# Optimization experiments

Hardware: AMD Instinct MI355X
Metric: run time of the kernel (lower is better)

Reference implementation:

```python
import jax, jax.numpy as jnp
import numpy as np

EMBED_DIM = 200
INPUT_DIM = 512


def setup_inputs() -> dict:
    key = jax.random.key(0)
    k1, k2, k3, k4 = jax.random.split(key, 4)
    B, L, T = 64, 256, 64
    x = jax.random.normal(k1, (B, L, INPUT_DIM), dtype=jnp.float32)
    y = jax.random.normal(k2, (B, T, INPUT_DIM), dtype=jnp.float32)
    # fc = nn.Linear(input_dim, embedding_dim)
    W = jax.random.normal(k3, (EMBED_DIM, INPUT_DIM), dtype=jnp.float32) * (1.0 / np.sqrt(INPUT_DIM))
    b = jax.random.normal(k4, (EMBED_DIM,), dtype=jnp.float32) * 0.01
    return {"x": x, "y": y, "W": W, "b": b}


def reference(x, y, W, b):
    # Project both modalities (last dim != embedding_dim in original triggers fc)
    xp = jnp.einsum('bld,ed->ble', x, W) + b   # B x L x E
    yp = jnp.einsum('btd,ed->bte', y, W) + b   # B x T x E
    # Pairwise matchmap: for pair (i, j), matchmap = xp[i] @ yp[j].T -> L x T
    mm = jnp.einsum('ile,jte->ijlt', xp, yp)   # B x B x L x T
    # MISA: max over L (rows of matchmap, dim 0), then mean over T
    S = jnp.max(mm, axis=2).mean(axis=2)       # B x B
    return S
```

## Files before the change

### kernel.cpp

```cpp
#include <hip/hip_runtime.h>
#include <hip/hip_bf16.h>
#include <stdint.h>

#define BB 64
#define LL 256
#define TT 64
#define DD 512
#define EE 200
#define EP 208
#define NKK 13
#define NROWS_X 16384
#define BSTRIDE 264
#define PBM 80

typedef __attribute__((ext_vector_type(8))) short short8;
typedef __attribute__((ext_vector_type(4))) float floatx4;
typedef __attribute__((ext_vector_type(16))) float floatx16;

__device__ __forceinline__ short f2bf(float f) {
  uint32_t u = __builtin_bit_cast(uint32_t, f);
  u = (u + 0x7fffu + ((u >> 16) & 1u)) >> 16;
  return (short)u;
}

__device__ __forceinline__ uint32_t pack2(float lo, float hi) {
  return __builtin_amdgcn_perm(__builtin_bit_cast(uint32_t, hi),
                               __builtin_bit_cast(uint32_t, lo), 0x07060302u);
}

typedef const __attribute__((address_space(1))) uint32_t gu32_t;
typedef __attribute__((address_space(3))) uint32_t lu32_t;
__device__ __forceinline__ void glds16(const void* g, void* l) {
  __builtin_amdgcn_global_load_lds((gu32_t*)g, (lu32_t*)l, 16, 0, 0);
}

#define VMCNT_BARRIER(N) asm volatile("s_waitcnt vmcnt(" #N ") lgkmcnt(0)\n\ts_barrier" ::: "memory")

__global__ void wcvt_kernel(const float* __restrict__ W, short* __restrict__ Wb) {
  const int t = blockIdx.x * 256 + threadIdx.x;
  const int base = t * 8;
  const int e = base >> 9;
  short8 o;
  if (e < EE) {
    const floatx4 f0 = *(const floatx4*)(W + base);
    const floatx4 f1 = *(const floatx4*)(W + base + 4);
    o[0] = f2bf(f0.x); o[1] = f2bf(f0.y); o[2] = f2bf(f0.z); o[3] = f2bf(f0.w);
    o[4] = f2bf(f1.x); o[5] = f2bf(f1.y); o[6] = f2bf(f1.z); o[7] = f2bf(f1.w);
  } else {
    o = (short8)0;
  }
  *(short8*)(Wb + base) = o;
}

__global__ __launch_bounds__(960, 1) void proj_kernel(const float* __restrict__ x,
                                                      const float* __restrict__ y,
                                                      const short* __restrict__ Wb,
                                                      const float* __restrict__ bias,
                                                      short* __restrict__ pT) {
  __shared__ __align__(16) char smem[70656];
  float* ldsA = (float*)smem;
  short* ldsB = (short*)(smem + 30720);
  short* bounce = (short*)smem;

  const int tid  = threadIdx.x;
  const int lane = tid & 63;
  const int wid  = tid >> 6;
  const int r16   = lane & 15;
  const int khalf = lane >> 4;
  const int mw = wid % 5;
  const int eh = wid / 5;
  const int nbase = (eh == 0) ? 0 : (eh == 1) ? 5 : 9;
  const int ncnt  = (eh == 0) ? 5 : 4;

  const int row0 = blockIdx.x * PBM;

  floatx4 acc[5];
#pragma unroll
  for (int n = 0; n < 5; n++) acc[n] = (floatx4){0.f, 0.f, 0.f, 0.f};

  auto stage = [&](int buf, int ks) {
    {
      if (tid < 640) {
        const int a = tid;
        const int r = a >> 3, c = a & 7;
        const int gr = row0 + r;
        const float* src = (gr < NROWS_X) ? (x + (size_t)gr * DD)
                                          : (y + (size_t)(gr - NROWS_X) * DD);
        glds16(src + ks * 32 + ((c ^ (r & 7)) << 2),
               &ldsA[buf * 2560 + a * 4]);
      } else {
        const int q = tid - 640;
        const int r = q >> 2, c = q & 3;
        glds16(Wb + (size_t)r * DD + ks * 32 + ((c ^ ((r >> 1) & 3)) << 3),
               &ldsB[buf * 6656 + q * 8]);
      }
    }
    {
      const int q = (tid < 512) ? (tid + 320) : (tid - 512);
      const int r = q >> 2, c = q & 3;
      glds16(Wb + (size_t)r * DD + ks * 32 + ((c ^ ((r >> 1) & 3)) << 3),
             &ldsB[buf * 6656 + q * 8]);
    }
  };

  auto compute = [&](int s) {
    const int buf = s % 3;
    const int r = mw * 16 + r16;
    const int c0 = (2 * khalf) ^ (r & 7);
    const int c1 = (2 * khalf + 1) ^ (r & 7);
    const floatx4 f0 = *(const floatx4*)&ldsA[buf * 2560 + r * 32 + c0 * 4];
    const floatx4 f1 = *(const floatx4*)&ldsA[buf * 2560 + r * 32 + c1 * 4];
    union { short8 s8; uint32_t u[4]; } af;
    af.u[0] = pack2(f0.x, f0.y);
    af.u[1] = pack2(f0.z, f0.w);
    af.u[2] = pack2(f1.x, f1.y);
    af.u[3] = pack2(f1.z, f1.w);
    const int bcol = (khalf ^ ((r16 >> 1) & 3)) << 3;
#pragma unroll
    for (int n = 0; n < 5; n++) {
      if (n < ncnt) {
        const int erow = (nbase + n) * 16 + r16;
        const short8 bfrag = *(const short8*)&ldsB[buf * 6656 + erow * 32 + bcol];
        acc[n] = __builtin_amdgcn_mfma_f32_16x16x32_bf16(af.s8, bfrag, acc[n], 0, 0, 0);
      }
    }
  };

  stage(0, 0);
  stage(1, 1);

  for (int s = 0; s < 15; s++) {
    VMCNT_BARRIER(2);
    if (s + 2 < 16) stage((s + 2) % 3, s + 2);
    compute(s);
  }
  VMCNT_BARRIER(0);
  compute(15);

  __syncthreads();

  for (int n = 0; n < ncnt; n++) {
    const int e = (nbase + n) * 16 + r16;
    const float bv = (e < EE) ? bias[e] : 0.0f;
#pragma unroll
    for (int rr = 0; rr < 4; rr++) {
      const int lr = mw * 16 + khalf * 4 + rr;
      bounce[lr * BSTRIDE + e] = f2bf(acc[n][rr] + bv);
    }
  }
  __syncthreads();

  for (int c = tid; c < 2080; c += 960) {
    const int n    = c / 160;
    const int rem  = c - n * 160;
    const int lrow = rem >> 1;
    const int ehh  = rem & 1;
    const int gr   = row0 + lrow;
    const short8 piece = *(const short8*)&bounce[lrow * BSTRIDE + n * 16 + ehh * 8];
    *(short8*)&pT[((size_t)((gr >> 5) * 13 + n)) * 512 + (size_t)(((ehh << 5) | (gr & 31)) * 8)] = piece;
  }
}

__global__ __launch_bounds__(512, 2) void pair_kernel(const short* __restrict__ xpT,
                                                      const short* __restrict__ ypT,
                                                      float* __restrict__ S) {
  __shared__ __align__(16) char lds[2 * 53248 + 16384];
  float* red = (float*)(lds + 2 * 53248);

  const int tid  = threadIdx.x;
  const int lane = tid & 63;
  const int wid  = tid >> 6;
  const int jj2  = wid >> 2;
  const int wj   = wid & 3;
  const int bid  = blockIdx.x;
  const int i    = bid & 63;
  const int jq   = bid >> 6;
  const int jbase = jq * 16;

  short8 a0[NKK], a1[NKK];
  {
    const short* ab0 = xpT + ((size_t)((i * 8 + wj * 2 + 0) * NKK)) * 512 + lane * 8;
    const short* ab1 = xpT + ((size_t)((i * 8 + wj * 2 + 1) * NKK)) * 512 + lane * 8;
#pragma unroll
    for (int kk = 0; kk < NKK; kk++) {
      a0[kk] = *(const short8*)(ab0 + kk * 512);
      a1[kk] = *(const short8*)(ab1 + kk * 512);
    }
  }

  auto stageB = [&](int g) {
    const short* src = ypT + (size_t)(jbase + g * 2) * 26 * 512;
    char* dst = lds + (g & 1) * 53248;
    for (int c = tid; c < 3328; c += 512)
      glds16(src + (size_t)c * 8, dst + c * 16);
  };

  stageB(0);
  __syncthreads();

  for (int g = 0; g < 8; g++) {
    if (g + 1 < 8) stageB(g + 1);

    const int j = g * 2 + jj2;
    const short* bbase = (const short*)(lds + (g & 1) * 53248) +
                         (size_t)(jj2 * 26 * 512) + lane * 8;

    floatx16 accA0n0, accA0n1, accA1n0, accA1n1;
#pragma unroll
    for (int r = 0; r < 16; r++) {
      accA0n0[r] = 0.f; accA0n1[r] = 0.f; accA1n0[r] = 0.f; accA1n1[r] = 0.f;
    }

#pragma unroll
    for (int kk = 0; kk < NKK; kk++) {
      const short8 b0 = *(const short8*)(bbase + (0 * NKK + kk) * 512);
      const short8 b1 = *(const short8*)(bbase + (1 * NKK + kk) * 512);
      accA0n0 = __builtin_amdgcn_mfma_f32_32x32x16_bf16(a0[kk], b0, accA0n0, 0, 0, 0);
      accA1n0 = __builtin_amdgcn_mfma_f32_32x32x16_bf16(a1[kk], b0, accA1n0, 0, 0, 0);
      accA0n1 = __builtin_amdgcn_mfma_f32_32x32x16_bf16(a0[kk], b1, accA0n1, 0, 0, 0);
      accA1n1 = __builtin_amdgcn_mfma_f32_32x32x16_bf16(a1[kk], b1, accA1n1, 0, 0, 0);
    }

    float v0 = accA0n0[0], v1 = accA0n1[0];
#pragma unroll
    for (int r = 0; r < 16; r++) {
      v0 = fmaxf(v0, accA0n0[r]); v0 = fmaxf(v0, accA1n0[r]);
      v1 = fmaxf(v1, accA0n1[r]); v1 = fmaxf(v1, accA1n1[r]);
    }
    v0 = fmaxf(v0, __shfl_xor(v0, 32, 64));
    v1 = fmaxf(v1, __shfl_xor(v1, 32, 64));
    if (lane < 32) {
      red[(j * 4 + wj) * 64 + 0 * 32 + lane] = v0;
      red[(j * 4 + wj) * 64 + 1 * 32 + lane] = v1;
    }

    __syncthreads();
  }

#pragma unroll
  for (int rep = 0; rep < 2; rep++) {
    const int j = wid * 2 + rep;
    const int t = lane;
    float v = red[(j * 4 + 0) * 64 + t];
    v = fmaxf(v, red[(j * 4 + 1) * 64 + t]);
    v = fmaxf(v, red[(j * 4 + 2) * 64 + t]);
    v = fmaxf(v, red[(j * 4 + 3) * 64 + t]);
    v += __shfl_xor(v, 1, 64);
    v += __shfl_xor(v, 2, 64);
    v += __shfl_xor(v, 4, 64);
    v += __shfl_xor(v, 8, 64);
    v += __shfl_xor(v, 16, 64);
    v += __shfl_xor(v, 32, 64);
    if (t == 0) S[i * BB + jbase + j] = v * (1.0f / 64.0f);
  }
}

extern "C" void kernel_launch(void* const* d_in, const int* in_sizes, int n_in,
                              void* d_out, int out_size, void* d_ws, size_t ws_size,
                              hipStream_t stream) {
  const float* x = (const float*)d_in[0];
  const float* y = (const float*)d_in[1];
  const float* W = (const float*)d_in[2];
  const float* b = (const float*)d_in[3];
  float* S = (float*)d_out;

  char* ws = (char*)d_ws;
  short* Wb = (short*)ws;
  short* pT = (short*)(ws + 262144);
  short* ypT = pT + (size_t)6656 * 512;

  wcvt_kernel<<<52, 256, 0, stream>>>(W, Wb);
  proj_kernel<<<256, 960, 0, stream>>>(x, y, Wb, b, pT);
  pair_kernel<<<256, 512, 0, stream>>>(pT, ypT, S);
}
```

Before: 44.96 us.

## Reassign pair-kernel blocks to two i rows per block and fix projection staging

```diff
diff --git a/kernel.cpp b/kernel.cpp
--- a/kernel.cpp
+++ b/kernel.cpp
@@ -95,8 +95,8 @@
                &ldsB[buf * 6656 + q * 8]);
       }
     }
-    {
-      const int q = (tid < 512) ? (tid + 320) : (tid - 512);
+    if (tid < 512) {
+      const int q = tid + 320;
       const int r = q >> 2, c = q & 3;
       glds16(Wb + (size_t)r * DD + ks * 32 + ((c ^ ((r >> 1) & 3)) << 3),
              &ldsB[buf * 6656 + q * 8]);
@@ -130,7 +130,7 @@
   stage(1, 1);
 
   for (int s = 0; s < 15; s++) {
-    VMCNT_BARRIER(2);
+    VMCNT_BARRIER(1);
     if (s + 2 < 16) stage((s + 2) % 3, s + 2);
     compute(s);
   }
@@ -161,7 +161,7 @@
   }
 }
 
-__global__ __launch_bounds__(512, 2) void pair_kernel(const short* __restrict__ xpT,
+__global__ __launch_bounds__(512, 1) void pair_kernel(const short* __restrict__ xpT,
                                                       const short* __restrict__ ypT,
                                                       float* __restrict__ S) {
   __shared__ __align__(16) char lds[2 * 53248 + 16384];
@@ -170,12 +170,13 @@
   const int tid  = threadIdx.x;
   const int lane = tid & 63;
   const int wid  = tid >> 6;
-  const int jj2  = wid >> 2;
+  const int il   = wid >> 2;
   const int wj   = wid & 3;
   const int bid  = blockIdx.x;
-  const int i    = bid & 63;
-  const int jq   = bid >> 6;
-  const int jbase = jq * 16;
+  const int ip   = bid & 31;
+  const int jo   = bid >> 5;
+  const int i    = ip * 2 + il;
+  const int j0   = jo * 8;
 
   short8 a0[NKK], a1[NKK];
   {
@@ -189,7 +190,7 @@
   }
 
   auto stageB = [&](int g) {
-    const short* src = ypT + (size_t)(jbase + g * 2) * 26 * 512;
+    const short* src = ypT + (size_t)(j0 + g * 2) * 26 * 512;
     char* dst = lds + (g & 1) * 53248;
     for (int c = tid; c < 3328; c += 512)
       glds16(src + (size_t)c * 8, dst + c * 16);
@@ -198,60 +199,64 @@
   stageB(0);
   __syncthreads();
 
-  for (int g = 0; g < 8; g++) {
-    if (g + 1 < 8) stageB(g + 1);
-
-    const int j = g * 2 + jj2;
-    const short* bbase = (const short*)(lds + (g & 1) * 53248) +
-                         (size_t)(jj2 * 26 * 512) + lane * 8;
-
-    floatx16 accA0n0, accA0n1, accA1n0, accA1n1;
-#pragma unroll
-    for (int r = 0; r < 16; r++) {
-      accA0n0[r] = 0.f; accA0n1[r] = 0.f; accA1n0[r] = 0.f; accA1n1[r] = 0.f;
-    }
-
-#pragma unroll
-    for (int kk = 0; kk < NKK; kk++) {
-      const short8 b0 = *(const short8*)(bbase + (0 * NKK + kk) * 512);
-      const short8 b1 = *(const short8*)(bbase + (1 * NKK + kk) * 512);
-      accA0n0 = __builtin_amdgcn_mfma_f32_32x32x16_bf16(a0[kk], b0, accA0n0, 0, 0, 0);
-      accA1n0 = __builtin_amdgcn_mfma_f32_32x32x16_bf16(a1[kk], b0, accA1n0, 0, 0, 0);
-      accA0n1 = __builtin_amdgcn_mfma_f32_32x32x16_bf16(a0[kk], b1, accA0n1, 0, 0, 0);
-      accA1n1 = __builtin_amdgcn_mfma_f32_32x32x16_bf16(a1[kk], b1, accA1n1, 0, 0, 0);
-    }
-
-    float v0 = accA0n0[0], v1 = accA0n1[0];
-#pragma unroll
-    for (int r = 0; r < 16; r++) {
-      v0 = fmaxf(v0, accA0n0[r]); v0 = fmaxf(v0, accA1n0[r]);
-      v1 = fmaxf(v1, accA0n1[r]); v1 = fmaxf(v1, accA1n1[r]);
-    }
-    v0 = fmaxf(v0, __shfl_xor(v0, 32, 64));
-    v1 = fmaxf(v1, __shfl_xor(v1, 32, 64));
-    if (lane < 32) {
-      red[(j * 4 + wj) * 64 + 0 * 32 + lane] = v0;
-      red[(j * 4 + wj) * 64 + 1 * 32 + lane] = v1;
-    }
-
+  for (int g = 0; g < 4; g++) {
+    if (g + 1 < 4) stageB(g + 1);
+
+#pragma unroll
+    for (int jj2 = 0; jj2 < 2; jj2++) {
+      const int j = g * 2 + jj2;
+      const short* bbase = (const short*)(lds + (g & 1) * 53248) +
+                           (size_t)(jj2 * 26 * 512) + lane * 8;
+
+      floatx16 acc00, acc01, acc10, acc11;
+#pragma unroll
+      for (int r = 0; r < 16; r++) {
+        acc00[r] = 0.f; acc01[r] = 0.f; acc10[r] = 0.f; acc11[r] = 0.f;
+      }
+
+#pragma unroll
+      for (int kk = 0; kk < NKK; kk++) {
+        const short8 b0 = *(const short8*)(bbase + (0 * NKK + kk) * 512);
+        const short8 b1 = *(const short8*)(bbase + (1 * NKK + kk) * 512);
+        acc00 = __builtin_amdgcn_mfma_f32_32x32x16_bf16(a0[kk], b0, acc00, 0, 0, 0);
+        acc10 = __builtin_amdgcn_mfma_f32_32x32x16_bf16(a1[kk], b0, acc10, 0, 0, 0);
+        acc01 = __builtin_amdgcn_mfma_f32_32x32x16_bf16(a0[kk], b1, acc01, 0, 0, 0);
+        acc11 = __builtin_amdgcn_mfma_f32_32x32x16_bf16(a1[kk], b1, acc11, 0, 0, 0);
+      }
+
+      float v0 = acc00[0], v1 = acc01[0];
+#pragma unroll
+      for (int r = 0; r < 16; r++) {
+        v0 = fmaxf(v0, acc00[r]); v0 = fmaxf(v0, acc10[r]);
+        v1 = fmaxf(v1, acc01[r]); v1 = fmaxf(v1, acc11[r]);
+      }
+      v0 = fmaxf(v0, __shfl_xor(v0, 32, 64));
+      v1 = fmaxf(v1, __shfl_xor(v1, 32, 64));
+      if (lane < 32) {
+        red[(((il * 8 + j) * 4 + wj)) * 64 + 0 * 32 + lane] = v0;
+        red[(((il * 8 + j) * 4 + wj)) * 64 + 1 * 32 + lane] = v1;
+      }
+    }
     __syncthreads();
   }
 
 #pragma unroll
   for (int rep = 0; rep < 2; rep++) {
-    const int j = wid * 2 + rep;
-    const int t = lane;
-    float v = red[(j * 4 + 0) * 64 + t];
-    v = fmaxf(v, red[(j * 4 + 1) * 64 + t]);
-    v = fmaxf(v, red[(j * 4 + 2) * 64 + t]);
-    v = fmaxf(v, red[(j * 4 + 3) * 64 + t]);
+    const int combo = wid * 2 + rep;
+    const int il2 = combo >> 3;
+    const int j   = combo & 7;
+    const int t   = lane;
+    float v = red[((il2 * 8 + j) * 4 + 0) * 64 + t];
+    v = fmaxf(v, red[((il2 * 8 + j) * 4 + 1) * 64 + t]);
+    v = fmaxf(v, red[((il2 * 8 + j) * 4 + 2) * 64 + t]);
+    v = fmaxf(v, red[((il2 * 8 + j) * 4 + 3) * 64 + t]);
     v += __shfl_xor(v, 1, 64);
     v += __shfl_xor(v, 2, 64);
     v += __shfl_xor(v, 4, 64);
     v += __shfl_xor(v, 8, 64);
     v += __shfl_xor(v, 16, 64);
     v += __shfl_xor(v, 32, 64);
-    if (t == 0) S[i * BB + jbase + j] = v * (1.0f / 64.0f);
+    if (t == 0) S[(ip * 2 + il2) * BB + j0 + j] = v * (1.0f / 64.0f);
   }
 }
 
```

After: 43.87 us (median of 2 runs). 2.4% less time.
